# Performance work log

Hardware: AMD Instinct MI355X
Metric: run time of the kernel (lower is better)

## Reference

```python
import jax, jax.numpy as jnp
import numpy as np

ALPHA = 0.2  # LeakyReLU negative slope
NEG = -9e15


def gat_layer(h, adj, W, a):
    # Faithful to the torch GAT: e_ij = leakyrelu(a^T [Wh_i || Wh_j])
    # = leakyrelu(a_src . Wh_i + a_dst . Wh_j); avoids the NxNx2F materialization.
    Wh = h @ W                              # [N, F]
    Fo = W.shape[1]
    a_src, a_dst = a[:Fo, 0], a[Fo:, 0]
    e = jax.nn.leaky_relu(
        (Wh @ a_src)[:, None] + (Wh @ a_dst)[None, :], negative_slope=ALPHA
    )                                        # [N, N]
    e = jnp.where(adj > 0, e, NEG)
    att = jax.nn.softmax(e, axis=1)          # dropout p=0 (eval)
    return jax.nn.elu(att @ Wh)


def gru_cell(x, h, W_ih, W_hh, b_ih, b_hh):
    # PyTorch GRUCell semantics.
    gi = x @ W_ih.T + b_ih                   # [N, 3F]
    gh = h @ W_hh.T + b_hh
    i_r, i_z, i_n = jnp.split(gi, 3, axis=1)
    h_r, h_z, h_n = jnp.split(gh, 3, axis=1)
    r = jax.nn.sigmoid(i_r + h_r)
    z = jax.nn.sigmoid(i_z + h_z)
    n = jnp.tanh(i_n + r * h_n)
    return (1.0 - z) * n + z * h


def setup_inputs() -> dict:
    key = jax.random.key(0)
    ks = jax.random.split(key, 10)
    N, nfeat, nhid, nout = 8192, 256, 128, 128
    x = jax.random.normal(ks[0], (N, nfeat), dtype=jnp.float32)
    # sparse random binary adjacency (~32 avg degree) + self loops
    adj = (jax.random.uniform(ks[1], (N, N)) < 0.004).astype(jnp.float32)
    adj = jnp.maximum(adj, jnp.eye(N, dtype=jnp.float32))
    h_prev = jnp.zeros((N, nout), dtype=jnp.float32)

    def xavier(k, shape, gain=1.414):
        fan_in, fan_out = shape[0], shape[1]
        b = gain * np.sqrt(6.0 / (fan_in + fan_out))
        return jax.random.uniform(k, shape, jnp.float32, -b, b)

    W1 = xavier(ks[2], (nfeat, nhid))
    a1 = xavier(ks[3], (2 * nhid, 1))
    W2 = xavier(ks[4], (nhid, nout))
    a2 = xavier(ks[5], (2 * nout, 1))
    s = 1.0 / np.sqrt(nout)
    W_ih = jax.random.uniform(ks[6], (3 * nout, nout), jnp.float32, -s, s)
    W_hh = jax.random.uniform(ks[7], (3 * nout, nout), jnp.float32, -s, s)
    b_ih = jax.random.uniform(ks[8], (3 * nout,), jnp.float32, -s, s)
    b_hh = jax.random.uniform(ks[9], (3 * nout,), jnp.float32, -s, s)
    return {"x": x, "adj": adj, "h_prev": h_prev, "W1": W1, "a1": a1,
            "W2": W2, "a2": a2, "W_ih": W_ih, "W_hh": W_hh,
            "b_ih": b_ih, "b_hh": b_hh}


def reference(x, adj, h_prev, W1, a1, W2, a2, W_ih, W_hh, b_ih, b_hh):
    x1 = gat_layer(x, adj, W1, a1)
    h_spat = gat_layer(x1, adj, W2, a2)
    return gru_cell(h_spat, h_prev, W_ih, W_hh, b_ih, b_hh)
```

## Files before the change

kernel.cpp:

```cpp
#include <hip/hip_runtime.h>
#include <math.h>

#define N_NODES 8192
#define CAP 128
#define LRELU_ALPHA 0.2f

typedef float v4f __attribute__((ext_vector_type(4)));

template <int K>
__device__ __forceinline__ void gemm_from_lds(
    int r0, int t, const float* As, const float* __restrict__ W,
    const float* __restrict__ a, float* __restrict__ Wh, float* __restrict__ src,
    float* __restrict__ dst, float (*red)[4][2]) {
  int c = t & 127, half = t >> 7;
  float acc[4] = {0.f, 0.f, 0.f, 0.f};
  const float* Asl = As + (half * 4) * K;
#pragma unroll 8
  for (int k = 0; k < K; k++) {
    float wv = W[k * 128 + c];
#pragma unroll
    for (int r = 0; r < 4; r++) acc[r] += Asl[r * K + k] * wv;
  }
  float as = a[c], ad = a[128 + c];
  int wv_id = t >> 6, lane = t & 63;
#pragma unroll
  for (int r = 0; r < 4; r++) {
    int row = half * 4 + r;
    Wh[(size_t)(r0 + row) * 128 + c] = acc[r];
    float s = acc[r] * as, d = acc[r] * ad;
#pragma unroll
    for (int off = 32; off; off >>= 1) {
      s += __shfl_xor(s, off);
      d += __shfl_xor(d, off);
    }
    if (lane == 0) { red[wv_id][r][0] = s; red[wv_id][r][1] = d; }
  }
  __syncthreads();
  if (t < 8) {
    int wa = (t < 4) ? 0 : 2, rr = t & 3;
    src[r0 + t] = red[wa][rr][0] + red[wa + 1][rr][0];
    dst[r0 + t] = red[wa][rr][1] + red[wa + 1][rr][1];
  }
}

__device__ __forceinline__ float2 agg_node_wave(
    int i, int lane, const float* __restrict__ Wh, const float* __restrict__ src,
    const float* __restrict__ dst, const int* __restrict__ idxbuf,
    const int* __restrict__ counts) {
  int c = counts[i];
  float si = src[i];
  int j0 = 0, j1 = 0;
  float e0 = -1e30f, e1 = -1e30f;
  if (lane < c) {
    j0 = idxbuf[(size_t)i * CAP + lane];
    float xv = si + dst[j0];
    e0 = xv > 0.f ? xv : LRELU_ALPHA * xv;
  }
  if (lane + 64 < c) {
    j1 = idxbuf[(size_t)i * CAP + lane + 64];
    float xv = si + dst[j1];
    e1 = xv > 0.f ? xv : LRELU_ALPHA * xv;
  }
  float m = fmaxf(e0, e1);
#pragma unroll
  for (int off = 32; off; off >>= 1) m = fmaxf(m, __shfl_xor(m, off));
  float w0 = (lane < c) ? expf(e0 - m) : 0.f;
  float w1 = (lane + 64 < c) ? expf(e1 - m) : 0.f;
  float s = w0 + w1;
#pragma unroll
  for (int off = 32; off; off >>= 1) s += __shfl_xor(s, off);
  float inv = 1.f / s;
  const float2* Wh2 = (const float2*)Wh;
  float ax = 0.f, ay = 0.f;
  int cc = c < 64 ? c : 64;
  int k = 0;
  for (; k + 3 < cc; k += 4) {
    float wa = __shfl(w0, k),     wb = __shfl(w0, k + 1);
    float wc_ = __shfl(w0, k + 2), wd = __shfl(w0, k + 3);
    int ja = __shfl(j0, k),     jb = __shfl(j0, k + 1);
    int jc = __shfl(j0, k + 2), jd = __shfl(j0, k + 3);
    float2 va = Wh2[ja * 64 + lane];
    float2 vb = Wh2[jb * 64 + lane];
    float2 vc = Wh2[jc * 64 + lane];
    float2 vd = Wh2[jd * 64 + lane];
    ax += wa * va.x + wb * vb.x + wc_ * vc.x + wd * vd.x;
    ay += wa * va.y + wb * vb.y + wc_ * vc.y + wd * vd.y;
  }
  for (; k < cc; k++) {
    float wk = __shfl(w0, k);
    int jk = __shfl(j0, k);
    float2 v = Wh2[jk * 64 + lane];
    ax += wk * v.x; ay += wk * v.y;
  }
  for (k = 64; k < c; k++) {
    float wk = __shfl(w1, k - 64);
    int jk = __shfl(j1, k - 64);
    float2 v = Wh2[jk * 64 + lane];
    ax += wk * v.x; ay += wk * v.y;
  }
  ax *= inv; ay *= inv;
  return make_float2(ax > 0.f ? ax : expf(ax) - 1.f,
                     ay > 0.f ? ay : expf(ay) - 1.f);
}

__global__ __launch_bounds__(256) void kA(
    const float* __restrict__ adj, int* __restrict__ idxbuf, int* __restrict__ counts,
    const float* __restrict__ x, const float* __restrict__ W1, const float* __restrict__ a1,
    float* __restrict__ Wh1, float* __restrict__ src1, float* __restrict__ dst1,
    const float* __restrict__ Wi, const float* __restrict__ Whm, float* __restrict__ WiT,
    float* __restrict__ WhT) {
  __shared__ float As[8 * 256];
  __shared__ float red[4][4][2];
  __shared__ int jn[CAP];
  __shared__ int cnt;
  int t = threadIdx.x, b = blockIdx.x;
  if (b < N_NODES) {
    if (t == 0) cnt = 0;
    __syncthreads();
    const v4f* row = (const v4f*)(adj + (size_t)b * N_NODES);
    v4f v[8];
#pragma unroll
    for (int u = 0; u < 8; u++) v[u] = __builtin_nontemporal_load(row + t + 256 * u);
#pragma unroll
    for (int u = 0; u < 8; u++) {
      int n = (v[u].x > 0.f) + (v[u].y > 0.f) + (v[u].z > 0.f) + (v[u].w > 0.f);
      if (n) {
        int p = atomicAdd(&cnt, n);
        int j0 = (t + 256 * u) * 4;
        if (v[u].x > 0.f) { if (p < CAP) jn[p] = j0;     p++; }
        if (v[u].y > 0.f) { if (p < CAP) jn[p] = j0 + 1; p++; }
        if (v[u].z > 0.f) { if (p < CAP) jn[p] = j0 + 2; p++; }
        if (v[u].w > 0.f) { if (p < CAP) jn[p] = j0 + 3; p++; }
      }
    }
    __syncthreads();
    int c = cnt > CAP ? CAP : cnt;
    if (t < c) idxbuf[(size_t)b * CAP + t] = jn[t];
    if (t == 0) counts[b] = c;
  } else if (b < N_NODES + 1024) {
    int tile = b - N_NODES;
    const float4* Ab4 = (const float4*)(x + (size_t)tile * 8 * 256);
    float4* As4 = (float4*)As;
#pragma unroll
    for (int l = t; l < 8 * 256 / 4; l += 256) As4[l] = Ab4[l];
    __syncthreads();
    gemm_from_lds<256>(tile * 8, t, As, W1, a1, Wh1, src1, dst1, red);
  } else {
    for (int n = (b - N_NODES - 1024) * 256 + t; n < 384 * 128; n += 64 * 256) {
      int r = n >> 7, c = n & 127;
      WiT[c * 384 + r] = Wi[n];
      WhT[c * 384 + r] = Whm[n];
    }
  }
}

__global__ __launch_bounds__(256) void kB(
    const float* __restrict__ Wh1, const float* __restrict__ src1,
    const float* __restrict__ dst1, const int* __restrict__ idxbuf,
    const int* __restrict__ counts, const float* __restrict__ W2, const float* __restrict__ a2,
    float* __restrict__ Wh2, float* __restrict__ src2, float* __restrict__ dst2) {
  __shared__ float tile[8 * 128];
  __shared__ float red[4][4][2];
  int t = threadIdx.x, b = blockIdx.x;
  int i0 = b * 8;
  int wv = t >> 6, lane = t & 63;
  float2 r0 = agg_node_wave(i0 + wv, lane, Wh1, src1, dst1, idxbuf, counts);
  *(float2*)&tile[wv * 128 + 2 * lane] = r0;
  float2 r1 = agg_node_wave(i0 + 4 + wv, lane, Wh1, src1, dst1, idxbuf, counts);
  *(float2*)&tile[(4 + wv) * 128 + 2 * lane] = r1;
  __syncthreads();
  gemm_from_lds<128>(i0, t, tile, W2, a2, Wh2, src2, dst2, red);
}

__global__ __launch_bounds__(256) void kC(
    const float* __restrict__ Wh2, const float* __restrict__ src2,
    const float* __restrict__ dst2, const int* __restrict__ idxbuf,
    const int* __restrict__ counts, const float* __restrict__ hprev,
    const float* __restrict__ WiT, const float* __restrict__ WhT,
    const float* __restrict__ b_ih, const float* __restrict__ b_hh, float* __restrict__ outp) {
  __shared__ float tile[8 * 128];
  __shared__ float hs[8 * 128];
  int t = threadIdx.x, b = blockIdx.x;
  int i0 = b * 8;
  ((float4*)hs)[t] = ((const float4*)(hprev + (size_t)i0 * 128))[t];
  int wv = t >> 6, lane = t & 63;
  float2 r0 = agg_node_wave(i0 + wv, lane, Wh2, src2, dst2, idxbuf, counts);
  *(float2*)&tile[wv * 128 + 2 * lane] = r0;
  float2 r1 = agg_node_wave(i0 + 4 + wv, lane, Wh2, src2, dst2, idxbuf, counts);
  *(float2*)&tile[(4 + wv) * 128 + 2 * lane] = r1;
  __syncthreads();
  int c = t & 127, half = t >> 7;
  const float* xsl = tile + half * 4 * 128;
  const float* hsl = hs + half * 4 * 128;
  float rg[4], zg[4];
  {
    float ai[4] = {0.f}, ah[4] = {0.f};
#pragma unroll 4
    for (int k = 0; k < 128; k++) {
      float wi = WiT[k * 384 + c], wh = WhT[k * 384 + c];
#pragma unroll
      for (int r = 0; r < 4; r++) { ai[r] += xsl[r * 128 + k] * wi; ah[r] += hsl[r * 128 + k] * wh; }
    }
    float bi = b_ih[c], bh = b_hh[c];
#pragma unroll
    for (int r = 0; r < 4; r++) rg[r] = 1.f / (1.f + expf(-(ai[r] + bi + ah[r] + bh)));
  }
  {
    float ai[4] = {0.f}, ah[4] = {0.f};
#pragma unroll 4
    for (int k = 0; k < 128; k++) {
      float wi = WiT[k * 384 + 128 + c], wh = WhT[k * 384 + 128 + c];
#pragma unroll
      for (int r = 0; r < 4; r++) { ai[r] += xsl[r * 128 + k] * wi; ah[r] += hsl[r * 128 + k] * wh; }
    }
    float bi = b_ih[128 + c], bh = b_hh[128 + c];
#pragma unroll
    for (int r = 0; r < 4; r++) zg[r] = 1.f / (1.f + expf(-(ai[r] + bi + ah[r] + bh)));
  }
  {
    float ai[4] = {0.f}, ah[4] = {0.f};
#pragma unroll 4
    for (int k = 0; k < 128; k++) {
      float wi = WiT[k * 384 + 256 + c], wh = WhT[k * 384 + 256 + c];
#pragma unroll
      for (int r = 0; r < 4; r++) { ai[r] += xsl[r * 128 + k] * wi; ah[r] += hsl[r * 128 + k] * wh; }
    }
    float bi = b_ih[256 + c], bh = b_hh[256 + c];
#pragma unroll
    for (int r = 0; r < 4; r++) {
      float n = tanhf(ai[r] + bi + rg[r] * (ah[r] + bh));
      outp[(size_t)(i0 + half * 4 + r) * 128 + c] =
          (1.f - zg[r]) * n + zg[r] * hsl[r * 128 + c];
    }
  }
}

extern "C" void kernel_launch(void* const* d_in, const int* in_sizes, int n_in,
                              void* d_out, int out_size, void* d_ws, size_t ws_size,
                              hipStream_t stream) {
  const float* x     = (const float*)d_in[0];
  const float* adj   = (const float*)d_in[1];
  const float* hprev = (const float*)d_in[2];
  const float* W1    = (const float*)d_in[3];
  const float* a1    = (const float*)d_in[4];
  const float* W2    = (const float*)d_in[5];
  const float* a2    = (const float*)d_in[6];
  const float* Wi    = (const float*)d_in[7];
  const float* Whm   = (const float*)d_in[8];
  const float* b_ih  = (const float*)d_in[9];
  const float* b_hh  = (const float*)d_in[10];
  float* outp = (float*)d_out;

  char* p = (char*)d_ws;
  float* Wh1    = (float*)p; p += (size_t)N_NODES * 128 * 4;
  float* Wh2    = (float*)p; p += (size_t)N_NODES * 128 * 4;
  float* src1   = (float*)p; p += (size_t)N_NODES * 4;
  float* dst1   = (float*)p; p += (size_t)N_NODES * 4;
  float* src2   = (float*)p; p += (size_t)N_NODES * 4;
  float* dst2   = (float*)p; p += (size_t)N_NODES * 4;
  float* WiT    = (float*)p; p += (size_t)384 * 128 * 4;
  float* WhT    = (float*)p; p += (size_t)384 * 128 * 4;
  int*   counts = (int*)p;   p += (size_t)N_NODES * 4;
  int*   idxbuf = (int*)p;   p += (size_t)N_NODES * CAP * 4;

  kA<<<N_NODES + 1024 + 64, 256, 0, stream>>>(adj, idxbuf, counts, x, W1, a1, Wh1, src1, dst1,
                                              Wi, Whm, WiT, WhT);
  kB<<<N_NODES / 8, 256, 0, stream>>>(Wh1, src1, dst1, idxbuf, counts, W2, a2, Wh2, src2, dst2);
  kC<<<N_NODES / 8, 256, 0, stream>>>(Wh2, src2, dst2, idxbuf, counts, hprev, WiT, WhT, b_ih,
                                      b_hh, outp);
}
```

Before: 448.6 us.

## Vectorize LDS reads, unroll neighbor gather by eight, fuse GRU gates, reorder kA blocks

```diff
diff --git a/kernel.cpp b/kernel.cpp
--- a/kernel.cpp
+++ b/kernel.cpp
@@ -15,11 +15,17 @@
   int c = t & 127, half = t >> 7;
   float acc[4] = {0.f, 0.f, 0.f, 0.f};
   const float* Asl = As + (half * 4) * K;
-#pragma unroll 8
-  for (int k = 0; k < K; k++) {
-    float wv = W[k * 128 + c];
-#pragma unroll
-    for (int r = 0; r < 4; r++) acc[r] += Asl[r * K + k] * wv;
+#pragma unroll 2
+  for (int k = 0; k < K; k += 4) {
+    float w0 = W[(k + 0) * 128 + c];
+    float w1 = W[(k + 1) * 128 + c];
+    float w2 = W[(k + 2) * 128 + c];
+    float w3 = W[(k + 3) * 128 + c];
+#pragma unroll
+    for (int r = 0; r < 4; r++) {
+      float4 av = *(const float4*)&Asl[r * K + k];
+      acc[r] += av.x * w0 + av.y * w1 + av.z * w2 + av.w * w3;
+    }
   }
   float as = a[c], ad = a[128 + c];
   int wv_id = t >> 6, lane = t & 63;
@@ -73,34 +79,67 @@
   const float2* Wh2 = (const float2*)Wh;
   float ax = 0.f, ay = 0.f;
   int cc = c < 64 ? c : 64;
-  int k = 0;
-  for (; k + 3 < cc; k += 4) {
-    float wa = __shfl(w0, k),     wb = __shfl(w0, k + 1);
-    float wc_ = __shfl(w0, k + 2), wd = __shfl(w0, k + 3);
-    int ja = __shfl(j0, k),     jb = __shfl(j0, k + 1);
-    int jc = __shfl(j0, k + 2), jd = __shfl(j0, k + 3);
-    float2 va = Wh2[ja * 64 + lane];
-    float2 vb = Wh2[jb * 64 + lane];
-    float2 vc = Wh2[jc * 64 + lane];
-    float2 vd = Wh2[jd * 64 + lane];
-    ax += wa * va.x + wb * vb.x + wc_ * vc.x + wd * vd.x;
-    ay += wa * va.y + wb * vb.y + wc_ * vc.y + wd * vd.y;
-  }
-  for (; k < cc; k++) {
-    float wk = __shfl(w0, k);
-    int jk = __shfl(j0, k);
-    float2 v = Wh2[jk * 64 + lane];
-    ax += wk * v.x; ay += wk * v.y;
-  }
-  for (k = 64; k < c; k++) {
-    float wk = __shfl(w1, k - 64);
-    int jk = __shfl(j1, k - 64);
-    float2 v = Wh2[jk * 64 + lane];
-    ax += wk * v.x; ay += wk * v.y;
+  for (int k = 0; k < cc; k += 8) {
+    float w_[8]; int j_[8]; float2 v_[8];
+#pragma unroll
+    for (int q = 0; q < 8; q++) { w_[q] = __shfl(w0, k + q); j_[q] = __shfl(j0, k + q); }
+#pragma unroll
+    for (int q = 0; q < 8; q++) v_[q] = Wh2[(size_t)j_[q] * 64 + lane];
+#pragma unroll
+    for (int q = 0; q < 8; q++) { ax += w_[q] * v_[q].x; ay += w_[q] * v_[q].y; }
+  }
+  if (c > 64) {
+    for (int k = 64; k < c; k++) {
+      float wk = __shfl(w1, k - 64);
+      int jk = __shfl(j1, k - 64);
+      float2 v = Wh2[(size_t)jk * 64 + lane];
+      ax += wk * v.x; ay += wk * v.y;
+    }
   }
   ax *= inv; ay *= inv;
   return make_float2(ax > 0.f ? ax : expf(ax) - 1.f,
                      ay > 0.f ? ay : expf(ay) - 1.f);
+}
+
+__device__ __forceinline__ void gru_tile(
+    int i0, int t, const float* tile, const float* hs, const float* __restrict__ WiT,
+    const float* __restrict__ WhT, const float* __restrict__ b_ih,
+    const float* __restrict__ b_hh, float* __restrict__ outp) {
+  int c = t & 127, half = t >> 7;
+  const float* xsl = tile + half * 4 * 128;
+  const float* hsl = hs + half * 4 * 128;
+  float ai[3][4] = {{0.f}}, ah[3][4] = {{0.f}};
+  for (int k = 0; k < 128; k += 4) {
+    float4 xv[4], hv[4];
+#pragma unroll
+    for (int r = 0; r < 4; r++) {
+      xv[r] = *(const float4*)&xsl[r * 128 + k];
+      hv[r] = *(const float4*)&hsl[r * 128 + k];
+    }
+#pragma unroll
+    for (int g = 0; g < 3; g++) {
+      int base = g * 128 + c;
+      float wi0 = WiT[(k + 0) * 384 + base], wi1 = WiT[(k + 1) * 384 + base];
+      float wi2 = WiT[(k + 2) * 384 + base], wi3 = WiT[(k + 3) * 384 + base];
+      float wh0 = WhT[(k + 0) * 384 + base], wh1 = WhT[(k + 1) * 384 + base];
+      float wh2 = WhT[(k + 2) * 384 + base], wh3 = WhT[(k + 3) * 384 + base];
+#pragma unroll
+      for (int r = 0; r < 4; r++) {
+        ai[g][r] += xv[r].x * wi0 + xv[r].y * wi1 + xv[r].z * wi2 + xv[r].w * wi3;
+        ah[g][r] += hv[r].x * wh0 + hv[r].y * wh1 + hv[r].z * wh2 + hv[r].w * wh3;
+      }
+    }
+  }
+  float bi0 = b_ih[c], bi1 = b_ih[128 + c], bi2 = b_ih[256 + c];
+  float bh0 = b_hh[c], bh1 = b_hh[128 + c], bh2 = b_hh[256 + c];
+#pragma unroll
+  for (int r = 0; r < 4; r++) {
+    float rg = 1.f / (1.f + expf(-(ai[0][r] + bi0 + ah[0][r] + bh0)));
+    float zg = 1.f / (1.f + expf(-(ai[1][r] + bi1 + ah[1][r] + bh1)));
+    float n = tanhf(ai[2][r] + bi2 + rg * (ah[2][r] + bh2));
+    outp[(size_t)(i0 + half * 4 + r) * 128 + c] =
+        (1.f - zg) * n + zg * hsl[r * 128 + c];
+  }
 }
 
 __global__ __launch_bounds__(256) void kA(
@@ -114,13 +153,27 @@
   __shared__ int jn[CAP];
   __shared__ int cnt;
   int t = threadIdx.x, b = blockIdx.x;
-  if (b < N_NODES) {
+  if (b < 1024) {
+    const float4* Ab4 = (const float4*)(x + (size_t)b * 8 * 256);
+    float4* As4 = (float4*)As;
+#pragma unroll
+    for (int l = t; l < 8 * 256 / 4; l += 256) As4[l] = Ab4[l];
+    __syncthreads();
+    gemm_from_lds<256>(b * 8, t, As, W1, a1, Wh1, src1, dst1, red);
+  } else if (b < 1088) {
+    for (int n = (b - 1024) * 256 + t; n < 384 * 128; n += 64 * 256) {
+      int r = n >> 7, c = n & 127;
+      WiT[c * 384 + r] = Wi[n];
+      WhT[c * 384 + r] = Whm[n];
+    }
+  } else {
+    int row = b - 1088;
     if (t == 0) cnt = 0;
     __syncthreads();
-    const v4f* row = (const v4f*)(adj + (size_t)b * N_NODES);
+    const v4f* rowp = (const v4f*)(adj + (size_t)row * N_NODES);
     v4f v[8];
 #pragma unroll
-    for (int u = 0; u < 8; u++) v[u] = __builtin_nontemporal_load(row + t + 256 * u);
+    for (int u = 0; u < 8; u++) v[u] = __builtin_nontemporal_load(rowp + t + 256 * u);
 #pragma unroll
     for (int u = 0; u < 8; u++) {
       int n = (v[u].x > 0.f) + (v[u].y > 0.f) + (v[u].z > 0.f) + (v[u].w > 0.f);
@@ -135,22 +188,8 @@
     }
     __syncthreads();
     int c = cnt > CAP ? CAP : cnt;
-    if (t < c) idxbuf[(size_t)b * CAP + t] = jn[t];
-    if (t == 0) counts[b] = c;
-  } else if (b < N_NODES + 1024) {
-    int tile = b - N_NODES;
-    const float4* Ab4 = (const float4*)(x + (size_t)tile * 8 * 256);
-    float4* As4 = (float4*)As;
-#pragma unroll
-    for (int l = t; l < 8 * 256 / 4; l += 256) As4[l] = Ab4[l];
-    __syncthreads();
-    gemm_from_lds<256>(tile * 8, t, As, W1, a1, Wh1, src1, dst1, red);
-  } else {
-    for (int n = (b - N_NODES - 1024) * 256 + t; n < 384 * 128; n += 64 * 256) {
-      int r = n >> 7, c = n & 127;
-      WiT[c * 384 + r] = Wi[n];
-      WhT[c * 384 + r] = Whm[n];
-    }
+    if (t < c) idxbuf[(size_t)row * CAP + t] = jn[t];
+    if (t == 0) counts[row] = c;
   }
 }
 
@@ -189,50 +228,7 @@
   float2 r1 = agg_node_wave(i0 + 4 + wv, lane, Wh2, src2, dst2, idxbuf, counts);
   *(float2*)&tile[(4 + wv) * 128 + 2 * lane] = r1;
   __syncthreads();
-  int c = t & 127, half = t >> 7;
-  const float* xsl = tile + half * 4 * 128;
-  const float* hsl = hs + half * 4 * 128;
-  float rg[4], zg[4];
-  {
-    float ai[4] = {0.f}, ah[4] = {0.f};
-#pragma unroll 4
-    for (int k = 0; k < 128; k++) {
-      float wi = WiT[k * 384 + c], wh = WhT[k * 384 + c];
-#pragma unroll
-      for (int r = 0; r < 4; r++) { ai[r] += xsl[r * 128 + k] * wi; ah[r] += hsl[r * 128 + k] * wh; }
-    }
-    float bi = b_ih[c], bh = b_hh[c];
-#pragma unroll
-    for (int r = 0; r < 4; r++) rg[r] = 1.f / (1.f + expf(-(ai[r] + bi + ah[r] + bh)));
-  }
-  {
-    float ai[4] = {0.f}, ah[4] = {0.f};
-#pragma unroll 4
-    for (int k = 0; k < 128; k++) {
-      float wi = WiT[k * 384 + 128 + c], wh = WhT[k * 384 + 128 + c];
-#pragma unroll
-      for (int r = 0; r < 4; r++) { ai[r] += xsl[r * 128 + k] * wi; ah[r] += hsl[r * 128 + k] * wh; }
-    }
-    float bi = b_ih[128 + c], bh = b_hh[128 + c];
-#pragma unroll
-    for (int r = 0; r < 4; r++) zg[r] = 1.f / (1.f + expf(-(ai[r] + bi + ah[r] + bh)));
-  }
-  {
-    float ai[4] = {0.f}, ah[4] = {0.f};
-#pragma unroll 4
-    for (int k = 0; k < 128; k++) {
-      float wi = WiT[k * 384 + 256 + c], wh = WhT[k * 384 + 256 + c];
-#pragma unroll
-      for (int r = 0; r < 4; r++) { ai[r] += xsl[r * 128 + k] * wi; ah[r] += hsl[r * 128 + k] * wh; }
-    }
-    float bi = b_ih[256 + c], bh = b_hh[256 + c];
-#pragma unroll
-    for (int r = 0; r < 4; r++) {
-      float n = tanhf(ai[r] + bi + rg[r] * (ah[r] + bh));
-      outp[(size_t)(i0 + half * 4 + r) * 128 + c] =
-          (1.f - zg[r]) * n + zg[r] * hsl[r * 128 + c];
-    }
-  }
+  gru_tile(i0, t, tile, hs, WiT, WhT, b_ih, b_hh, outp);
 }
 
 extern "C" void kernel_launch(void* const* d_in, const int* in_sizes, int n_in,
@@ -263,7 +259,7 @@
   int*   counts = (int*)p;   p += (size_t)N_NODES * 4;
   int*   idxbuf = (int*)p;   p += (size_t)N_NODES * CAP * 4;
 
-  kA<<<N_NODES + 1024 + 64, 256, 0, stream>>>(adj, idxbuf, counts, x, W1, a1, Wh1, src1, dst1,
+  kA<<<1024 + 64 + N_NODES, 256, 0, stream>>>(adj, idxbuf, counts, x, W1, a1, Wh1, src1, dst1,
                                               Wi, Whm, WiT, WhT);
   kB<<<N_NODES / 8, 256, 0, stream>>>(Wh1, src1, dst1, idxbuf, counts, W2, a2, Wh2, src2, dst2);
   kC<<<N_NODES / 8, 256, 0, stream>>>(Wh2, src2, dst2, idxbuf, counts, hprev, WiT, WhT, b_ih,
```

New measurement: 432.2 us. 3.7% less time.
